# Kernel optimization log

Measured on AMD Instinct MI355X. Metric: run time of the kernel, lower is better.

Reference implementation:

```python
import jax, jax.numpy as jnp
import numpy as np

KH, KW = 3, 3
STRIDE, PAD, DIL = 1, 1, 1


def setup_inputs() -> dict:
    key = jax.random.key(0)
    k1, k2, k3, k4 = jax.random.split(key, 4)
    B, C, H, W = 4, 256, 64, 64
    O = 256
    x = jax.random.normal(k1, (B, C, H, W), dtype=jnp.float32)
    offset = jax.random.normal(k2, (B, 2 * KH * KW, H, W), dtype=jnp.float32)
    mask = jax.random.uniform(k3, (B, KH * KW, H, W), dtype=jnp.float32)
    weight = jax.random.normal(k4, (O, C, KH, KW), dtype=jnp.float32) * 0.02
    bias = jnp.zeros((O,), dtype=jnp.float32)
    return {"x": x, "offset": offset, "mask": mask, "weight": weight, "bias": bias}


def _bilinear_sample(x, py, px):
    # x: [B,C,H,W]; py,px: [B,K,Ho,Wo] fractional sample coords (zero outside)
    B, C, H, W = x.shape
    y0 = jnp.floor(py)
    x0 = jnp.floor(px)
    ly, lx = py - y0, px - x0
    hy, hx = 1.0 - ly, 1.0 - lx
    y0i = y0.astype(jnp.int32)
    x0i = x0.astype(jnp.int32)
    xf = x.reshape(B, C, H * W)

    def gather(yi, xi):
        valid = (yi >= 0) & (yi < H) & (xi >= 0) & (xi < W)
        yc = jnp.clip(yi, 0, H - 1)
        xc = jnp.clip(xi, 0, W - 1)
        idx = yc * W + xc  # [B,K,Ho,Wo]
        g = jax.vmap(lambda xb, ib: xb[:, ib.reshape(-1)])(xf, idx)  # [B,C,K*Ho*Wo]
        g = g.reshape(B, C, *yi.shape[1:])
        return g * valid[:, None].astype(x.dtype)

    return (gather(y0i, x0i) * (hy * hx)[:, None]
            + gather(y0i, x0i + 1) * (hy * lx)[:, None]
            + gather(y0i + 1, x0i) * (ly * hx)[:, None]
            + gather(y0i + 1, x0i + 1) * (ly * lx)[:, None])


def reference(x, offset, mask, weight, bias):
    B, C, H, W = x.shape
    O = weight.shape[0]
    K = KH * KW
    Ho = (H + 2 * PAD - DIL * (KH - 1) - 1) // STRIDE + 1
    Wo = (W + 2 * PAD - DIL * (KW - 1) - 1) // STRIDE + 1
    off = offset.reshape(B, K, 2, Ho, Wo)
    tap_y = (jnp.repeat(jnp.arange(KH), KW) * DIL).astype(x.dtype)  # [K]
    tap_x = (jnp.tile(jnp.arange(KW), KH) * DIL).astype(x.dtype)
    base_y = (jnp.arange(Ho) * STRIDE - PAD).astype(x.dtype)  # [Ho]
    base_x = (jnp.arange(Wo) * STRIDE - PAD).astype(x.dtype)
    py = off[:, :, 0] + base_y[None, None, :, None] + tap_y[None, :, None, None]
    px = off[:, :, 1] + base_x[None, None, None, :] + tap_x[None, :, None, None]
    # sampled columns: [B,C,K,Ho,Wo], modulated by mask
    val = _bilinear_sample(x, py, px) * mask[:, None]
    out = jnp.einsum('bckhw,ock->bohw', val, weight.reshape(O, C, K))
    return out + bias[None, :, None, None]
```

## Files before the change

### kernel.cpp

```cpp
#include <hip/hip_runtime.h>

typedef _Float16 f16x8 __attribute__((ext_vector_type(8)));
typedef float f32x4 __attribute__((ext_vector_type(4)));

__device__ __forceinline__ unsigned short f2h(float f) {
  union { _Float16 h; unsigned short u; } v;
  v.h = (_Float16)f;
  return v.u;
}
__device__ __forceinline__ f16x8 splat8(float w) {
  _Float16 h = (_Float16)w;
  f16x8 v = {h, h, h, h, h, h, h, h};
  return v;
}

__global__ __launch_bounds__(256) void prep_wx(
    const float* __restrict__ x, const float* __restrict__ w,
    unsigned short* __restrict__ xt, uint4* __restrict__ wfrag) {
  const int bid = blockIdx.x;
  const int t = threadIdx.x;
  if (bid >= 1024) {
    const int idx = (bid - 1024) * 256 + t;
    const int l = idx & 63;
    const int kt = (idx >> 6) % 72;
    const int g = idx / (72 * 64);
    const int o = g * 16 + (l & 15);
    const int kbase = kt * 32 + ((l >> 4) * 8);
    unsigned short h[8];
#pragma unroll
    for (int e = 0; e < 8; ++e) {
      const int klin = kbase + e;
      const int kk = klin >> 8;
      const int c = klin & 255;
      h[e] = f2h(w[((size_t)o * 256 + c) * 9 + kk]);
    }
    uint4 p;
    p.x = (unsigned)h[0] | ((unsigned)h[1] << 16);
    p.y = (unsigned)h[2] | ((unsigned)h[3] << 16);
    p.z = (unsigned)h[4] | ((unsigned)h[5] << 16);
    p.w = (unsigned)h[6] | ((unsigned)h[7] << 16);
    wfrag[idx] = p;
    return;
  }
  const int b = bid >> 8;
  const int h = (bid >> 2) & 63;
  const int cq = bid & 3;
  const int wave = t >> 6, lane = t & 63;
  __shared__ float lds[64][65];
  const int wpos = t >> 2, sub = t & 3;
  const int cl0 = wave * 4 + (lane >> 4);
  const int w0 = (lane & 15) * 4;
#pragma unroll
  for (int iter = 0; iter < 4; ++iter) {
    const int cl = iter * 16 + cl0;
    const int c = cq * 64 + cl;
    float4 v = *(const float4*)(x + (((size_t)b * 256 + c) * 64 + h) * 64 + w0);
    lds[cl][w0] = v.x; lds[cl][w0 + 1] = v.y;
    lds[cl][w0 + 2] = v.z; lds[cl][w0 + 3] = v.w;
  }
  __syncthreads();
  unsigned short hb[16];
#pragma unroll
  for (int j = 0; j < 16; ++j) hb[j] = f2h(lds[sub * 16 + j][wpos]);
  uint4 p0, p1;
  p0.x = (unsigned)hb[0] | ((unsigned)hb[1] << 16);
  p0.y = (unsigned)hb[2] | ((unsigned)hb[3] << 16);
  p0.z = (unsigned)hb[4] | ((unsigned)hb[5] << 16);
  p0.w = (unsigned)hb[6] | ((unsigned)hb[7] << 16);
  p1.x = (unsigned)hb[8] | ((unsigned)hb[9] << 16);
  p1.y = (unsigned)hb[10] | ((unsigned)hb[11] << 16);
  p1.z = (unsigned)hb[12] | ((unsigned)hb[13] << 16);
  p1.w = (unsigned)hb[14] | ((unsigned)hb[15] << 16);
  unsigned short* dst = xt + (((size_t)b * 64 + h) * 64 + wpos) * 256 + cq * 64 + sub * 16;
  *(uint4*)dst = p0;
  *(uint4*)(dst + 8) = p1;
}

__device__ __forceinline__ void combine8(uint4 q0, uint4 q1, uint4 q2, uint4 q3,
                                         float4 wt, _Float16* dst) {
  f16x8 t0, t1, t2, t3;
  __builtin_memcpy(&t0, &q0, 16);
  __builtin_memcpy(&t1, &q1, 16);
  __builtin_memcpy(&t2, &q2, 16);
  __builtin_memcpy(&t3, &q3, 16);
  f16x8 r = t0 * splat8(wt.x);
  r += t1 * splat8(wt.y);
  r += t2 * splat8(wt.z);
  r += t3 * splat8(wt.w);
  __builtin_memcpy(dst, &r, 16);
}

__global__ __launch_bounds__(512, 2) void dcn_fused(
    const unsigned short* __restrict__ xt, const float* __restrict__ off,
    const float* __restrict__ mask, const uint4* __restrict__ wfrag,
    const float* __restrict__ bias, float* __restrict__ out) {
  __shared__ __align__(16) _Float16 Bs[2][4096];
  __shared__ __align__(16) float swt[9 * 64 * 4];
  __shared__ __align__(16) int sidx[9 * 64 * 4];

  const int bid = blockIdx.x;
  const int id = ((bid & 7) << 5) | (bid >> 3);
  const int b = id >> 6;
  const int nt = id & 63;

  const int tid = threadIdx.x;
  const int lane = tid & 63;
  const int wv = tid >> 6;
  const int lh = lane & 15, lg = lane >> 4;

  for (int pair = tid; pair < 576; pair += 512) {
    const int k = pair >> 6;
    const int pl = pair & 63;
    float oy = off[(((size_t)b * 18 + 2 * k) * 64 + nt) * 64 + pl];
    float ox = off[(((size_t)b * 18 + 2 * k + 1) * 64 + nt) * 64 + pl];
    float m = mask[(((size_t)b * 9 + k) * 64 + nt) * 64 + pl];
    float py = oy + (float)(nt - 1 + k / 3);
    float px = ox + (float)(pl - 1 + k % 3);
    float y0f = floorf(py), x0f = floorf(px);
    float ly = py - y0f, lx = px - x0f;
    float hy = 1.f - ly, hx = 1.f - lx;
    int y0 = (int)y0f, x0 = (int)x0f;
    int y1 = y0 + 1, x1 = x0 + 1;
    bool vy0 = (y0 >= 0) && (y0 < 64);
    bool vy1 = (y1 >= 0) && (y1 < 64);
    bool vx0 = (x0 >= 0) && (x0 < 64);
    bool vx1 = (x1 >= 0) && (x1 < 64);
    int yc0 = min(max(y0, 0), 63), yc1 = min(max(y1, 0), 63);
    int xc0 = min(max(x0, 0), 63), xc1 = min(max(x1, 0), 63);
    int* sp = sidx + (k * 64 + pl) * 4;
    float* wp = swt + (k * 64 + pl) * 4;
    sp[0] = (yc0 * 64 + xc0) * 256;
    sp[1] = (yc0 * 64 + xc1) * 256;
    sp[2] = (yc1 * 64 + xc0) * 256;
    sp[3] = (yc1 * 64 + xc1) * 256;
    wp[0] = (vy0 && vx0) ? hy * hx * m : 0.f;
    wp[1] = (vy0 && vx1) ? hy * lx * m : 0.f;
    wp[2] = (vy1 && vx0) ? ly * hx * m : 0.f;
    wp[3] = (vy1 && vx1) ? ly * lx * m : 0.f;
  }

  const uint4* aBase = wfrag + (size_t)(wv * 2) * 72 * 64 + lane;

  const int pos = tid >> 3, ci = tid & 7;
  const unsigned short* xtb = xt + (size_t)b * 1048576 + ci * 8;
  const int bsw = (ci >> 2) * 2048 + pos * 32 + (((ci & 3) ^ ((pos >> 1) & 3)) * 8);

  const int csw = (lg ^ ((lh >> 1) & 3)) * 8;
  int boff[4];
#pragma unroll
  for (int fn = 0; fn < 4; ++fn) boff[fn] = (fn * 16 + lh) * 32 + csw;

#define LOADA(P, AR)                                                               \
  do {                                                                             \
    _Pragma("unroll") for (int j = 0; j < 4; ++j)                                  \
        AR[j] = aBase[(size_t)((((j & 1) * 72) + 2 * (P) + (j >> 1)) * 64)];       \
  } while (0)

#define LOADTAPS(Q0, Q1, Q2, Q3, IX, CO)                                           \
  do {                                                                             \
    Q0 = *(const uint4*)(xtb + (IX).x + (CO));                                     \
    Q1 = *(const uint4*)(xtb + (IX).y + (CO));                                     \
    Q2 = *(const uint4*)(xtb + (IX).z + (CO));                                     \
    Q3 = *(const uint4*)(xtb + (IX).w + (CO));                                     \
  } while (0)

#define MFMA_PHASE(BUF, AR)                                                        \
  do {                                                                             \
    const _Float16* Bb = &Bs[BUF][0];                                              \
    f16x8 b0[4], b1[4];                                                            \
    _Pragma("unroll") for (int fn = 0; fn < 4; ++fn) {                             \
      b0[fn] = *(const f16x8*)(Bb + boff[fn]);                                     \
      b1[fn] = *(const f16x8*)(Bb + 2048 + boff[fn]);                              \
    }                                                                              \
    __builtin_amdgcn_s_setprio(1);                                                 \
    _Pragma("unroll") for (int fm = 0; fm < 2; ++fm)                               \
        _Pragma("unroll") for (int fn = 0; fn < 4; ++fn) {                         \
      acc[fm][fn] = __builtin_amdgcn_mfma_f32_16x16x32_f16(                        \
          *(const f16x8*)&AR[fm], b0[fn], acc[fm][fn], 0, 0, 0);                   \
      acc[fm][fn] = __builtin_amdgcn_mfma_f32_16x16x32_f16(                        \
          *(const f16x8*)&AR[2 + fm], b1[fn], acc[fm][fn], 0, 0, 0);               \
    }                                                                              \
    __builtin_amdgcn_s_setprio(0);                                                 \
  } while (0)

#define BAR()                                                                      \
  do {                                                                             \
    asm volatile("s_waitcnt lgkmcnt(0)" ::: "memory");                             \
    __builtin_amdgcn_sched_barrier(0);                                             \
    __builtin_amdgcn_s_barrier();                                                  \
    __builtin_amdgcn_sched_barrier(0);                                             \
  } while (0)

#define PHASE(P_, AL, AC, QL0, QL1, QL2, QL3, QC0, QC1, QC2, QC3)                  \
  do {                                                                             \
    LOADA((P_) + 1, AL);                                                           \
    int4 ix = *(const int4*)(sidx + ((((P_) + 2) >> 2) * 64 + pos) * 4);           \
    LOADTAPS(QL0, QL1, QL2, QL3, ix, (((P_) + 2) & 3) * 64);                       \
    float4 wt4 = *(const float4*)(swt + ((((P_) + 1) >> 2) * 64 + pos) * 4);       \
    MFMA_PHASE((P_) & 1, AC);                                                      \
    combine8(QC0, QC1, QC2, QC3, wt4, &Bs[((P_) + 1) & 1][0] + bsw);               \
    BAR();                                                                         \
  } while (0)

  f32x4 acc[2][4] = {};
  uint4 AE[4], AO[4];
  uint4 qA0, qA1, qA2, qA3, qB0, qB1, qB2, qB3;

  __syncthreads();

  {
    float4 wt0 = *(const float4*)(swt + pos * 4);
    int4 ix0 = *(const int4*)(sidx + pos * 4);
    LOADTAPS(qA0, qA1, qA2, qA3, ix0, 0);
    combine8(qA0, qA1, qA2, qA3, wt0, &Bs[0][0] + bsw);
    LOADA(0, AE);
    LOADTAPS(qB0, qB1, qB2, qB3, ix0, 64);
    BAR();
  }

  for (int p = 0; p < 34; p += 2) {
    PHASE(p, AO, AE, qA0, qA1, qA2, qA3, qB0, qB1, qB2, qB3);
    PHASE(p + 1, AE, AO, qB0, qB1, qB2, qB3, qA0, qA1, qA2, qA3);
  }
  {
    LOADA(35, AO);
    float4 wt4 = *(const float4*)(swt + (8 * 64 + pos) * 4);
    MFMA_PHASE(0, AE);
    combine8(qB0, qB1, qB2, qB3, wt4, &Bs[1][0] + bsw);
    BAR();
    MFMA_PHASE(1, AO);
  }

  float* outb = out + (size_t)b * 1048576 + (size_t)nt * 64;
#pragma unroll
  for (int fm = 0; fm < 2; ++fm) {
#pragma unroll
    for (int i = 0; i < 4; ++i) {
      const int o = wv * 32 + fm * 16 + lg * 4 + i;
      const float bs = bias[o];
      float* orow = outb + (size_t)o * 4096 + lh;
#pragma unroll
      for (int fn = 0; fn < 4; ++fn) orow[fn * 16] = acc[fm][fn][i] + bs;
    }
  }
#undef LOADA
#undef LOADTAPS
#undef MFMA_PHASE
#undef BAR
#undef PHASE
}

extern "C" void kernel_launch(void* const* d_in, const int* in_sizes, int n_in,
                              void* d_out, int out_size, void* d_ws, size_t ws_size,
                              hipStream_t stream) {
  const float* x = (const float*)d_in[0];
  const float* off = (const float*)d_in[1];
  const float* mask = (const float*)d_in[2];
  const float* wgt = (const float*)d_in[3];
  const float* bias = (const float*)d_in[4];
  float* out = (float*)d_out;

  uint4* wfrag = (uint4*)d_ws;
  unsigned short* xtp = (unsigned short*)(wfrag + 73728);

  prep_wx<<<1312, 256, 0, stream>>>(x, wgt, xtp, wfrag);
  dcn_fused<<<256, 512, 0, stream>>>(xtp, off, mask, wfrag, bias, out);
}
```

Baseline: 45.20 us.

## Process two K-tiles per barrier with four-slot LDS ring buffer

Restructures the main loop so that each barrier interval covers two 32-wide K tiles instead of one. Shared B staging grows from two to four buffers, and A fragments are double-buffered in groups of eight registers. This halves the number of workgroup barriers and lets tap gathers run further ahead of use. The cost is more LDS (an extra 16KB), more registers for A fragments, and a different ordering of loads relative to the MFMAs, which may hurt occupancy at 2 blocks per CU.

After: 45.25 us. About the same (+0.1%).

```diff
diff --git a/kernel.cpp b/kernel.cpp
--- a/kernel.cpp
+++ b/kernel.cpp
@@ -94,7 +94,7 @@
     const unsigned short* __restrict__ xt, const float* __restrict__ off,
     const float* __restrict__ mask, const uint4* __restrict__ wfrag,
     const float* __restrict__ bias, float* __restrict__ out) {
-  __shared__ __align__(16) _Float16 Bs[2][4096];
+  __shared__ __align__(16) _Float16 Bs[4][4096];
   __shared__ __align__(16) float swt[9 * 64 * 4];
   __shared__ __align__(16) int sidx[9 * 64 * 4];
 
@@ -150,23 +150,31 @@
 #pragma unroll
   for (int fn = 0; fn < 4; ++fn) boff[fn] = (fn * 16 + lh) * 32 + csw;
 
-#define LOADA(P, AR)                                                               \
+#define LOADA(T, AR4)                                                              \
   do {                                                                             \
     _Pragma("unroll") for (int j = 0; j < 4; ++j)                                  \
-        AR[j] = aBase[(size_t)((((j & 1) * 72) + 2 * (P) + (j >> 1)) * 64)];       \
-  } while (0)
-
-#define LOADTAPS(Q0, Q1, Q2, Q3, IX, CO)                                           \
-  do {                                                                             \
-    Q0 = *(const uint4*)(xtb + (IX).x + (CO));                                     \
-    Q1 = *(const uint4*)(xtb + (IX).y + (CO));                                     \
-    Q2 = *(const uint4*)(xtb + (IX).z + (CO));                                     \
-    Q3 = *(const uint4*)(xtb + (IX).w + (CO));                                     \
-  } while (0)
-
-#define MFMA_PHASE(BUF, AR)                                                        \
-  do {                                                                             \
-    const _Float16* Bb = &Bs[BUF][0];                                              \
+        (AR4)[j] = aBase[(size_t)((((j & 1) * 72) + 2 * (T) + (j >> 1)) * 64)];    \
+  } while (0)
+
+#define LOADTAPS(T, Q0, Q1, Q2, Q3)                                                \
+  do {                                                                             \
+    int4 ix = *(const int4*)(sidx + (((T) >> 2) * 64 + pos) * 4);                  \
+    const int co = ((T) & 3) * 64;                                                 \
+    Q0 = *(const uint4*)(xtb + ix.x + co);                                         \
+    Q1 = *(const uint4*)(xtb + ix.y + co);                                         \
+    Q2 = *(const uint4*)(xtb + ix.z + co);                                         \
+    Q3 = *(const uint4*)(xtb + ix.w + co);                                         \
+  } while (0)
+
+#define COMBINE(T, Q0, Q1, Q2, Q3)                                                 \
+  do {                                                                             \
+    float4 wt4 = *(const float4*)(swt + (((T) >> 2) * 64 + pos) * 4);              \
+    combine8(Q0, Q1, Q2, Q3, wt4, &Bs[(T) & 3][0] + bsw);                          \
+  } while (0)
+
+#define MFMA_T(T, AR4)                                                             \
+  do {                                                                             \
+    const _Float16* Bb = &Bs[(T) & 3][0];                                          \
     f16x8 b0[4], b1[4];                                                            \
     _Pragma("unroll") for (int fn = 0; fn < 4; ++fn) {                             \
       b0[fn] = *(const f16x8*)(Bb + boff[fn]);                                     \
@@ -176,9 +184,9 @@
     _Pragma("unroll") for (int fm = 0; fm < 2; ++fm)                               \
         _Pragma("unroll") for (int fn = 0; fn < 4; ++fn) {                         \
       acc[fm][fn] = __builtin_amdgcn_mfma_f32_16x16x32_f16(                        \
-          *(const f16x8*)&AR[fm], b0[fn], acc[fm][fn], 0, 0, 0);                   \
+          *(const f16x8*)&(AR4)[fm], b0[fn], acc[fm][fn], 0, 0, 0);                \
       acc[fm][fn] = __builtin_amdgcn_mfma_f32_16x16x32_f16(                        \
-          *(const f16x8*)&AR[2 + fm], b1[fn], acc[fm][fn], 0, 0, 0);               \
+          *(const f16x8*)&(AR4)[2 + fm], b1[fn], acc[fm][fn], 0, 0, 0);            \
     }                                                                              \
     __builtin_amdgcn_s_setprio(0);                                                 \
   } while (0)
@@ -191,45 +199,52 @@
     __builtin_amdgcn_sched_barrier(0);                                             \
   } while (0)
 
-#define PHASE(P_, AL, AC, QL0, QL1, QL2, QL3, QC0, QC1, QC2, QC3)                  \
-  do {                                                                             \
-    LOADA((P_) + 1, AL);                                                           \
-    int4 ix = *(const int4*)(sidx + ((((P_) + 2) >> 2) * 64 + pos) * 4);           \
-    LOADTAPS(QL0, QL1, QL2, QL3, ix, (((P_) + 2) & 3) * 64);                       \
-    float4 wt4 = *(const float4*)(swt + ((((P_) + 1) >> 2) * 64 + pos) * 4);       \
-    MFMA_PHASE((P_) & 1, AC);                                                      \
-    combine8(QC0, QC1, QC2, QC3, wt4, &Bs[((P_) + 1) & 1][0] + bsw);               \
+#define SUPER(S_, ACUR, ANXT)                                                      \
+  do {                                                                             \
+    MFMA_T(2 * (S_), ACUR);                                                        \
+    MFMA_T(2 * (S_) + 1, (ACUR) + 4);                                              \
+    LOADA(2 * (S_) + 2, ANXT);                                                     \
+    LOADA(2 * (S_) + 3, (ANXT) + 4);                                               \
+    COMBINE(2 * (S_) + 2, qA0, qA1, qA2, qA3);                                     \
+    LOADTAPS(2 * (S_) + 4, qA0, qA1, qA2, qA3);                                    \
+    COMBINE(2 * (S_) + 3, qB0, qB1, qB2, qB3);                                     \
+    LOADTAPS(2 * (S_) + 5, qB0, qB1, qB2, qB3);                                    \
     BAR();                                                                         \
   } while (0)
 
   f32x4 acc[2][4] = {};
-  uint4 AE[4], AO[4];
+  uint4 AE[8], AO[8];
   uint4 qA0, qA1, qA2, qA3, qB0, qB1, qB2, qB3;
 
   __syncthreads();
 
   {
-    float4 wt0 = *(const float4*)(swt + pos * 4);
-    int4 ix0 = *(const int4*)(sidx + pos * 4);
-    LOADTAPS(qA0, qA1, qA2, qA3, ix0, 0);
-    combine8(qA0, qA1, qA2, qA3, wt0, &Bs[0][0] + bsw);
+    LOADTAPS(0, qA0, qA1, qA2, qA3);
+    LOADTAPS(1, qB0, qB1, qB2, qB3);
+    COMBINE(0, qA0, qA1, qA2, qA3);
+    COMBINE(1, qB0, qB1, qB2, qB3);
     LOADA(0, AE);
-    LOADTAPS(qB0, qB1, qB2, qB3, ix0, 64);
+    LOADA(1, AE + 4);
+    LOADTAPS(2, qA0, qA1, qA2, qA3);
+    LOADTAPS(3, qB0, qB1, qB2, qB3);
     BAR();
   }
 
-  for (int p = 0; p < 34; p += 2) {
-    PHASE(p, AO, AE, qA0, qA1, qA2, qA3, qB0, qB1, qB2, qB3);
-    PHASE(p + 1, AE, AO, qB0, qB1, qB2, qB3, qA0, qA1, qA2, qA3);
+  for (int s = 0; s < 16; s += 2) {
+    SUPER(s, AE, AO);
+    SUPER(s + 1, AO, AE);
   }
   {
-    LOADA(35, AO);
-    float4 wt4 = *(const float4*)(swt + (8 * 64 + pos) * 4);
-    MFMA_PHASE(0, AE);
-    combine8(qB0, qB1, qB2, qB3, wt4, &Bs[1][0] + bsw);
+    MFMA_T(32, AE);
+    MFMA_T(33, AE + 4);
+    LOADA(34, AO);
+    LOADA(35, AO + 4);
+    COMBINE(34, qA0, qA1, qA2, qA3);
+    COMBINE(35, qB0, qB1, qB2, qB3);
     BAR();
-    MFMA_PHASE(1, AO);
-  }
+  }
+  MFMA_T(34, AO);
+  MFMA_T(35, AO + 4);
 
   float* outb = out + (size_t)b * 1048576 + (size_t)nt * 64;
 #pragma unroll
@@ -245,9 +260,10 @@
   }
 #undef LOADA
 #undef LOADTAPS
-#undef MFMA_PHASE
+#undef COMBINE
+#undef MFMA_T
 #undef BAR
-#undef PHASE
+#undef SUPER
 }
 
 extern "C" void kernel_launch(void* const* d_in, const int* in_sizes, int n_in,
```
